# Optimization experiments

Measured on AMD Instinct MI355X. Metric: run time of the kernel, lower is better.

Reference implementation:

```python
import jax, jax.numpy as jnp
import numpy as np

EMBED_DIM = 1024
NUM_HEADS = 16
HEAD_DIM = EMBED_DIM // NUM_HEADS
NUM_GLOBAL = 2
NUM_RANDOM = 3
WINDOW_SIZE = 3
B, S = 2, 2048


def setup_inputs() -> dict:
    key = jax.random.key(0)
    ks = jax.random.split(key, 10)
    scale = 0.02
    inp = {
        "x": jax.random.normal(ks[0], (B, S, EMBED_DIM), dtype=jnp.float32),
        "random_indices": jax.random.randint(ks[1], (S, NUM_RANDOM), 0, S, dtype=jnp.int32),
        "q_w": jax.random.normal(ks[2], (EMBED_DIM, EMBED_DIM), dtype=jnp.float32) * scale,
        "q_b": jnp.zeros((EMBED_DIM,), dtype=jnp.float32),
        "k_w": jax.random.normal(ks[3], (EMBED_DIM, EMBED_DIM), dtype=jnp.float32) * scale,
        "k_b": jnp.zeros((EMBED_DIM,), dtype=jnp.float32),
        "v_w": jax.random.normal(ks[4], (EMBED_DIM, EMBED_DIM), dtype=jnp.float32) * scale,
        "v_b": jnp.zeros((EMBED_DIM,), dtype=jnp.float32),
        "o_w": jax.random.normal(ks[5], (EMBED_DIM, EMBED_DIM), dtype=jnp.float32) * scale,
        "o_b": jnp.zeros((EMBED_DIM,), dtype=jnp.float32),
    }
    return inp


def _build_mask(random_indices, seq_len):
    # [S, S] boolean BigBird mask: global rows/cols + sliding window + random.
    i = jnp.arange(seq_len)[:, None]
    j = jnp.arange(seq_len)[None, :]
    glob = (i < NUM_GLOBAL) | (j < NUM_GLOBAL)
    win = jnp.abs(i - j) <= WINDOW_SIZE
    rand = jnp.zeros((seq_len, seq_len), dtype=bool)
    rows = jnp.repeat(jnp.arange(seq_len), NUM_RANDOM)
    rand = rand.at[rows, random_indices.reshape(-1)].set(True)
    return glob | win | rand


def reference(x, random_indices, q_w, q_b, k_w, k_b, v_w, v_b, o_w, o_b):
    b, s, _ = x.shape
    # torch nn.Linear: y = x @ W.T + b
    q = (x @ q_w.T + q_b).reshape(b, s, NUM_HEADS, HEAD_DIM).transpose(0, 2, 1, 3)
    k = (x @ k_w.T + k_b).reshape(b, s, NUM_HEADS, HEAD_DIM).transpose(0, 2, 1, 3)
    v = (x @ v_w.T + v_b).reshape(b, s, NUM_HEADS, HEAD_DIM).transpose(0, 2, 1, 3)
    scores = jnp.einsum("bhqd,bhkd->bhqk", q, k) / jnp.sqrt(jnp.float32(HEAD_DIM))
    mask = _build_mask(random_indices, s)  # [S, S]
    scores = jnp.where(mask[None, None, :, :], scores, -jnp.inf)
    probs = jax.nn.softmax(scores, axis=-1)
    out = jnp.einsum("bhqk,bhkd->bhqd", probs, v)
    out = out.transpose(0, 2, 1, 3).reshape(b, s, EMBED_DIM)
    return out @ o_w.T + o_b
```

## Files before the change

kernel.cpp:

```cpp
#include <hip/hip_runtime.h>

#define B_  2
#define S_  2048
#define E_  1024
#define H_  16
#define D_  64
#define NGLOB 2
#define NRAND 3
#define WIN 3

typedef __bf16 bf16x8 __attribute__((ext_vector_type(8)));
typedef float  f32x4  __attribute__((ext_vector_type(4)));

__device__ __forceinline__ unsigned short f2bf(float f) {
    unsigned u = __builtin_bit_cast(unsigned, f);
    unsigned r = u + 0x7FFFu + ((u >> 16) & 1u);
    return (unsigned short)(r >> 16);
}
__device__ __forceinline__ float bf2f(unsigned short u) {
    return __builtin_bit_cast(float, (unsigned)u << 16);
}

__device__ __forceinline__ void g2l16(const unsigned short* g, unsigned short* l) {
    __builtin_amdgcn_global_load_lds(
        (const __attribute__((address_space(1))) unsigned*)g,
        (__attribute__((address_space(3))) unsigned*)l, 16, 0, 0);
}

__global__ __launch_bounds__(256)
void convert_all(const float* __restrict__ x,  const float* __restrict__ qw,
                 const float* __restrict__ kw, const float* __restrict__ vw,
                 const float* __restrict__ ow,
                 unsigned short* __restrict__ xb, unsigned short* __restrict__ wqkv,
                 unsigned short* __restrict__ wo) {
    const int XN = (B_ * S_ * E_) / 4;
    const int WN = (E_ * E_) / 4;
    int i = blockIdx.x * blockDim.x + threadIdx.x;
    int r, loc;
    if (i < XN) { r = 0; loc = i; }
    else        { int j = i - XN; r = 1 + (j >> 18); loc = j & (WN - 1); }
    const float* src = r == 0 ? x : r == 1 ? qw : r == 2 ? kw : r == 3 ? vw : ow;
    float4 f = ((const float4*)src)[loc];
    ushort4 u;
    u.x = f2bf(f.x); u.y = f2bf(f.y); u.z = f2bf(f.z); u.w = f2bf(f.w);
    ushort4* dst = r == 0 ? (ushort4*)xb : r == 4 ? (ushort4*)wo
                 : (ushort4*)wqkv + (size_t)(r - 1) * WN;
    dst[loc] = u;
}

__global__ __launch_bounds__(256, 4)
void gemm_qkv(const unsigned short* __restrict__ A,
              const unsigned short* __restrict__ W,
              const float* __restrict__ b0, const float* __restrict__ b1,
              const float* __restrict__ b2,
              unsigned short* __restrict__ Cb, int M, int N, int K) {
    __shared__ unsigned short sA[128 * 64];
    __shared__ unsigned short sB[128 * 64];
    const int t = threadIdx.x;
    const int lane = t & 63;
    const int wave = t >> 6;
    const int wm = wave >> 1, wn = wave & 1;
    const int lq = lane >> 4;
    const int lr = lane & 15;
    const int bm = blockIdx.x * 128;
    const int bn = blockIdx.y * 128;

    f32x4 acc[4][4] = {};

    for (int k0 = 0; k0 < K; k0 += 64) {
        const unsigned short* Abase = A + (size_t)bm * K + k0;
        const unsigned short* Wbase = W + (size_t)bn * K + k0;
        #pragma unroll
        for (int j = 0; j < 4; ++j) {
            int c = j * 256 + t;
            int row = c >> 3, cc = c & 7;
            int gcol = ((cc ^ (row & 7)) << 3);
            int dst = j * 2048 + wave * 512;
            g2l16(Abase + (size_t)row * K + gcol, sA + dst);
            g2l16(Wbase + (size_t)row * K + gcol, sB + dst);
        }
        __syncthreads();

        #pragma unroll
        for (int ks = 0; ks < 2; ++ks) {
            const int sw = (((ks << 2) + lq) ^ (lr & 7)) << 3;
            bf16x8 af[4], bfr[4];
            #pragma unroll
            for (int i = 0; i < 4; ++i)
                af[i] = *(const bf16x8*)&sA[(wm * 64 + i * 16 + lr) * 64 + sw];
            #pragma unroll
            for (int j = 0; j < 4; ++j)
                bfr[j] = *(const bf16x8*)&sB[(wn * 64 + j * 16 + lr) * 64 + sw];
            #pragma unroll
            for (int i = 0; i < 4; ++i)
                #pragma unroll
                for (int j = 0; j < 4; ++j)
                    acc[i][j] = __builtin_amdgcn_mfma_f32_16x16x32_bf16(af[i], bfr[j], acc[i][j], 0, 0, 0);
        }
        __syncthreads();
    }

    #pragma unroll
    for (int i = 0; i < 4; ++i) {
        int row0 = bm + wm * 64 + i * 16 + lq * 4;
        #pragma unroll
        for (int j = 0; j < 4; ++j) {
            int col = bn + wn * 64 + j * 16 + lr;
            const float* bp = col < E_ ? b0 : (col < 2 * E_ ? b1 : b2);
            float bv = bp[col & (E_ - 1)];
            #pragma unroll
            for (int r = 0; r < 4; ++r)
                Cb[(size_t)(row0 + r) * N + col] = f2bf(acc[i][j][r] + bv);
        }
    }
}

__global__ __launch_bounds__(256, 3)
void gemm_o(unsigned short* A,
            const unsigned short* __restrict__ W,
            const float* __restrict__ bias,
            const float* __restrict__ gaccp, const float* __restrict__ gms,
            float* __restrict__ Cf, int M, int N, int K) {
    __shared__ unsigned short sA[128 * 64];
    __shared__ unsigned short sB[128 * 64];
    const int t = threadIdx.x;
    const int lane = t & 63;
    const int wave = t >> 6;
    const int wm = wave >> 1, wn = wave & 1;
    const int lq = lane >> 4;
    const int lr = lane & 15;
    const int bm = blockIdx.x * 128;
    const int bn = blockIdx.y * 128;

    if (blockIdx.x == 0 || blockIdx.x == 16) {
        int b = blockIdx.x >> 4;
        #pragma unroll
        for (int r = 0; r < 8; ++r) {
            int oid = r * 256 + t;
            int i2 = oid >> 10, col = oid & 1023;
            int h = col >> 6, d = col & 63;
            int tup = b * 32 + i2 * 16 + h;
            float Mx = -1e30f;
            #pragma unroll
            for (int c = 0; c < 8; ++c) Mx = fmaxf(Mx, gms[(tup * 8 + c) * 2]);
            float den = 0.f, num = 0.f;
            #pragma unroll
            for (int c = 0; c < 8; ++c) {
                float f = __expf(gms[(tup * 8 + c) * 2] - Mx);
                den += gms[(tup * 8 + c) * 2 + 1] * f;
                num += gaccp[(size_t)(tup * 8 + c) * D_ + d] * f;
            }
            A[(size_t)(b * S_ + i2) * E_ + col] = f2bf(num / den);
        }
        asm volatile("s_waitcnt vmcnt(0)" ::: "memory");
    }
    __syncthreads();

    f32x4 acc[4][4] = {};

    for (int k0 = 0; k0 < K; k0 += 64) {
        const unsigned short* Abase = A + (size_t)bm * K + k0;
        const unsigned short* Wbase = W + (size_t)bn * K + k0;
        #pragma unroll
        for (int j = 0; j < 4; ++j) {
            int c = j * 256 + t;
            int row = c >> 3, cc = c & 7;
            int gcol = ((cc ^ (row & 7)) << 3);
            int dst = j * 2048 + wave * 512;
            g2l16(Abase + (size_t)row * K + gcol, sA + dst);
            g2l16(Wbase + (size_t)row * K + gcol, sB + dst);
        }
        __syncthreads();

        #pragma unroll
        for (int ks = 0; ks < 2; ++ks) {
            const int sw = (((ks << 2) + lq) ^ (lr & 7)) << 3;
            bf16x8 af[4], bfr[4];
            #pragma unroll
            for (int i = 0; i < 4; ++i)
                af[i] = *(const bf16x8*)&sA[(wm * 64 + i * 16 + lr) * 64 + sw];
            #pragma unroll
            for (int j = 0; j < 4; ++j)
                bfr[j] = *(const bf16x8*)&sB[(wn * 64 + j * 16 + lr) * 64 + sw];
            #pragma unroll
            for (int i = 0; i < 4; ++i)
                #pragma unroll
                for (int j = 0; j < 4; ++j)
                    acc[i][j] = __builtin_amdgcn_mfma_f32_16x16x32_bf16(af[i], bfr[j], acc[i][j], 0, 0, 0);
        }
        __syncthreads();
    }

    #pragma unroll
    for (int i = 0; i < 4; ++i) {
        int row0 = bm + wm * 64 + i * 16 + lq * 4;
        #pragma unroll
        for (int j = 0; j < 4; ++j) {
            int col = bn + wn * 64 + j * 16 + lr;
            float bv = bias[col];
            #pragma unroll
            for (int r = 0; r < 4; ++r)
                Cf[(size_t)(row0 + r) * N + col] = acc[i][j][r] + bv;
        }
    }
}

__global__ __launch_bounds__(256)
void attn_fused(const unsigned short* __restrict__ qkv,
                const int* __restrict__ rnd,
                float* __restrict__ gaccp, float* __restrict__ gms,
                unsigned short* __restrict__ attn) {
    const int NB = B_ * (S_ - 2);
    int t = threadIdx.x;

    if (blockIdx.x < 512) {
        int tup = blockIdx.x >> 3, seg = blockIdx.x & 7;
        int b = tup >> 5, i = (tup >> 4) & 1, h = tup & 15;
        int w = t >> 6, l = t & 63;
        __shared__ float redm[4], reds[4];
        __shared__ float ov[4][D_];

        const bf16x8* qp = (const bf16x8*)(qkv + (size_t)(b * S_ + i) * 3072 + h * D_);
        bf16x8 qv = qp[l & 7];
        float qreg[8];
        #pragma unroll
        for (int j = 0; j < 8; ++j) qreg[j] = (float)qv[j];

        const int key0 = seg * 256 + w * 64;
        const int ksb = l >> 3, dg = l & 7;
        float mM = -1e30f, ssum = 0.f;
        float o[8] = {};
        #pragma unroll
        for (int it = 0; it < 8; ++it) {
            int key = key0 + it * 8 + ksb;
            const unsigned short* kr =
                qkv + (size_t)(b * S_ + key) * 3072 + E_ + h * D_ + dg * 8;
            bf16x8 kv = *(const bf16x8*)kr;
            bf16x8 vv = *(const bf16x8*)(kr + E_);
            float s = 0.f;
            #pragma unroll
            for (int j = 0; j < 8; ++j) s += qreg[j] * (float)kv[j];
            s += __shfl_xor(s, 1);
            s += __shfl_xor(s, 2);
            s += __shfl_xor(s, 4);
            s *= 0.125f;
            float m_it = s;
            m_it = fmaxf(m_it, __shfl_xor(m_it, 8));
            m_it = fmaxf(m_it, __shfl_xor(m_it, 16));
            m_it = fmaxf(m_it, __shfl_xor(m_it, 32));
            if (m_it > mM) {
                float r = __expf(mM - m_it);
                ssum *= r;
                #pragma unroll
                for (int e2 = 0; e2 < 8; ++e2) o[e2] *= r;
                mM = m_it;
            }
            float e = __expf(s - mM);
            ssum += e;
            #pragma unroll
            for (int e2 = 0; e2 < 8; ++e2) o[e2] += e * (float)vv[e2];
        }
        #pragma unroll
        for (int mask = 8; mask <= 32; mask <<= 1) {
            ssum += __shfl_xor(ssum, mask);
            #pragma unroll
            for (int e2 = 0; e2 < 8; ++e2) o[e2] += __shfl_xor(o[e2], mask);
        }
        if (l == 0) { redm[w] = mM; reds[w] = ssum; }
        if (ksb == 0)
            #pragma unroll
            for (int e2 = 0; e2 < 8; ++e2) ov[w][dg * 8 + e2] = o[e2];
        __syncthreads();
        if (w == 0) {
            float M = fmaxf(fmaxf(redm[0], redm[1]), fmaxf(redm[2], redm[3]));
            float f0 = __expf(redm[0] - M), f1 = __expf(redm[1] - M);
            float f2 = __expf(redm[2] - M), f3 = __expf(redm[3] - M);
            gaccp[((size_t)tup * 8 + seg) * D_ + l] =
                ov[0][l] * f0 + ov[1][l] * f1 + ov[2][l] * f2 + ov[3][l] * f3;
            if (l == 0) {
                gms[(tup * 8 + seg) * 2]     = M;
                gms[(tup * 8 + seg) * 2 + 1] =
                    reds[0] * f0 + reds[1] * f1 + reds[2] * f2 + reds[3] * f3;
            }
        }
        return;
    }

    int bb = blockIdx.x - 512;
    int bidx = (bb & 7) * 128 + (bb >> 3);
    int w = t >> 6, l = t & 63;
    int row = bidx * 4 + w;
    bool valid = row < NB;
    int b = row / (S_ - 2);
    int i = row % (S_ - 2) + 2;
    if (!valid) { b = 0; i = 2; }

    __shared__ int cols_s[4][12];
    __shared__ int ncol_sh[4];

    const bf16x8* qp = (const bf16x8*)(qkv + (size_t)(b * S_ + i) * 3072);
    bf16x8 q0 = qp[l * 2], q1 = qp[l * 2 + 1];
    float qreg[16];
    #pragma unroll
    for (int j = 0; j < 8; ++j) { qreg[j] = (float)q0[j]; qreg[8 + j] = (float)q1[j]; }

    if (l == 0) {
        int* cols = cols_s[w];
        int n = 0;
        cols[n++] = 0; cols[n++] = 1;
        int lo = i - WIN; if (lo < NGLOB) lo = NGLOB;
        int hi = i + WIN; if (hi > S_ - 1) hi = S_ - 1;
        for (int j = lo; j <= hi; ++j) cols[n++] = j;
        for (int r = 0; r < NRAND; ++r) {
            int c = rnd[i * NRAND + r];
            bool dup = false;
            for (int q = 0; q < n; ++q) dup = dup || (cols[q] == c);
            if (!dup) cols[n++] = c;
        }
        ncol_sh[w] = n;
        for (int q = n; q < 12; ++q) cols[q] = 0;
    }
    __syncthreads();
    const int n = ncol_sh[w];

    float mM = -1e30f, ssum = 0.f;
    float o[16] = {};
    #pragma unroll
    for (int c = 0; c < 12; ++c) {
        const unsigned short* base = qkv + (size_t)(b * S_ + cols_s[w][c]) * 3072 + E_;
        const bf16x8* kp = (const bf16x8*)base;
        bf16x8 k0 = kp[l * 2], k1 = kp[l * 2 + 1];
        const bf16x8* vp = (const bf16x8*)(base + E_);
        bf16x8 v0 = vp[l * 2], v1 = vp[l * 2 + 1];
        float s = 0.f;
        #pragma unroll
        for (int j = 0; j < 8; ++j) s += qreg[j] * (float)k0[j] + qreg[8 + j] * (float)k1[j];
        s += __shfl_xor(s, 1);
        s += __shfl_xor(s, 2);
        s = (c < n) ? s * 0.125f : -1e30f;
        if (s > mM) {
            float r = __expf(mM - s);
            ssum *= r;
            #pragma unroll
            for (int j = 0; j < 16; ++j) o[j] *= r;
            mM = s;
        }
        float e = __expf(s - mM);
        ssum += e;
        #pragma unroll
        for (int j = 0; j < 8; ++j) { o[j] += e * (float)v0[j]; o[8 + j] += e * (float)v1[j]; }
    }
    float inv = 1.f / ssum;
    #pragma unroll
    for (int j = 0; j < 16; ++j) o[j] *= inv;

    if (valid) {
        ushort4 u0, u1, u2, u3;
        u0.x = f2bf(o[0]);  u0.y = f2bf(o[1]);  u0.z = f2bf(o[2]);  u0.w = f2bf(o[3]);
        u1.x = f2bf(o[4]);  u1.y = f2bf(o[5]);  u1.z = f2bf(o[6]);  u1.w = f2bf(o[7]);
        u2.x = f2bf(o[8]);  u2.y = f2bf(o[9]);  u2.z = f2bf(o[10]); u2.w = f2bf(o[11]);
        u3.x = f2bf(o[12]); u3.y = f2bf(o[13]); u3.z = f2bf(o[14]); u3.w = f2bf(o[15]);
        ushort4* op = (ushort4*)(attn + (size_t)(b * S_ + i) * E_ + l * 16);
        op[0] = u0; op[1] = u1; op[2] = u2; op[3] = u3;
    }
}

extern "C" void kernel_launch(void* const* d_in, const int* in_sizes, int n_in,
                              void* d_out, int out_size, void* d_ws, size_t ws_size,
                              hipStream_t stream) {
    const float* x   = (const float*)d_in[0];
    const int*   rnd = (const int*)d_in[1];
    const float* qw  = (const float*)d_in[2];
    const float* qb  = (const float*)d_in[3];
    const float* kw  = (const float*)d_in[4];
    const float* kb  = (const float*)d_in[5];
    const float* vw  = (const float*)d_in[6];
    const float* vb  = (const float*)d_in[7];
    const float* ow  = (const float*)d_in[8];
    const float* ob  = (const float*)d_in[9];
    float* out = (float*)d_out;

    char* ws = (char*)d_ws;
    unsigned short* xb    = (unsigned short*)(ws);
    unsigned short* wqkv  = (unsigned short*)(ws + 8388608);
    unsigned short* wo    = (unsigned short*)(ws + 14680064);
    unsigned short* qkv   = (unsigned short*)(ws + 16777216);
    unsigned short* attn  = (unsigned short*)(ws + 41943040);
    float*          gaccp = (float*)(ws);
    float*          gms   = (float*)(ws + 131072);

    const int M = B_ * S_;

    {
        int total4 = (M * E_ + 4 * E_ * E_) / 4;
        convert_all<<<total4 / 256, 256, 0, stream>>>(x, qw, kw, vw, ow, xb, wqkv, wo);
    }

    {
        dim3 grid(M / 128, 3 * E_ / 128);
        gemm_qkv<<<grid, 256, 0, stream>>>(xb, wqkv, qb, kb, vb, qkv, M, 3 * E_, E_);
    }

    attn_fused<<<512 + 1024, 256, 0, stream>>>(qkv, rnd, gaccp, gms, attn);

    {
        dim3 grid(M / 128, E_ / 128);
        gemm_o<<<grid, 256, 0, stream>>>(attn, wo, ob, gaccp, gms, out, M, E_, E_);
    }
}
```

Before: 160.1 us.

## Split attention key loops across two wavefronts per row with LDS merge

Doubles the attention block to 512 threads. Global-query blocks now have each wave cover 32 keys instead of 64, and the results of 8 waves are merged. Sparse rows are now handled by two waves, each processing half of the 12 candidate columns, with the partial softmax states combined through shared memory. This shortens each wave's serial latency-bound loop and exposes more memory parallelism, at the cost of an extra LDS round trip, a barrier, and more threads per block.

```diff
diff --git a/kernel.cpp b/kernel.cpp
--- a/kernel.cpp
+++ b/kernel.cpp
@@ -205,20 +205,20 @@
     }
 }
 
-__global__ __launch_bounds__(256)
+__global__ __launch_bounds__(512)
 void attn_fused(const unsigned short* __restrict__ qkv,
                 const int* __restrict__ rnd,
                 float* __restrict__ gaccp, float* __restrict__ gms,
                 unsigned short* __restrict__ attn) {
     const int NB = B_ * (S_ - 2);
     int t = threadIdx.x;
+    int w = t >> 6, l = t & 63;
 
     if (blockIdx.x < 512) {
         int tup = blockIdx.x >> 3, seg = blockIdx.x & 7;
         int b = tup >> 5, i = (tup >> 4) & 1, h = tup & 15;
-        int w = t >> 6, l = t & 63;
-        __shared__ float redm[4], reds[4];
-        __shared__ float ov[4][D_];
+        __shared__ float redm[8], reds[8];
+        __shared__ float ov[8][D_];
 
         const bf16x8* qp = (const bf16x8*)(qkv + (size_t)(b * S_ + i) * 3072 + h * D_);
         bf16x8 qv = qp[l & 7];
@@ -226,12 +226,12 @@
         #pragma unroll
         for (int j = 0; j < 8; ++j) qreg[j] = (float)qv[j];
 
-        const int key0 = seg * 256 + w * 64;
+        const int key0 = seg * 256 + w * 32;
         const int ksb = l >> 3, dg = l & 7;
         float mM = -1e30f, ssum = 0.f;
         float o[8] = {};
         #pragma unroll
-        for (int it = 0; it < 8; ++it) {
+        for (int it = 0; it < 4; ++it) {
             int key = key0 + it * 8 + ksb;
             const unsigned short* kr =
                 qkv + (size_t)(b * S_ + key) * 3072 + E_ + h * D_ + dg * 8;
@@ -272,15 +272,20 @@
             for (int e2 = 0; e2 < 8; ++e2) ov[w][dg * 8 + e2] = o[e2];
         __syncthreads();
         if (w == 0) {
-            float M = fmaxf(fmaxf(redm[0], redm[1]), fmaxf(redm[2], redm[3]));
-            float f0 = __expf(redm[0] - M), f1 = __expf(redm[1] - M);
-            float f2 = __expf(redm[2] - M), f3 = __expf(redm[3] - M);
-            gaccp[((size_t)tup * 8 + seg) * D_ + l] =
-                ov[0][l] * f0 + ov[1][l] * f1 + ov[2][l] * f2 + ov[3][l] * f3;
+            float M = -1e30f;
+            #pragma unroll
+            for (int ww = 0; ww < 8; ++ww) M = fmaxf(M, redm[ww]);
+            float num = 0.f, den = 0.f;
+            #pragma unroll
+            for (int ww = 0; ww < 8; ++ww) {
+                float f = __expf(redm[ww] - M);
+                num += ov[ww][l] * f;
+                den += reds[ww] * f;
+            }
+            gaccp[((size_t)tup * 8 + seg) * D_ + l] = num;
             if (l == 0) {
                 gms[(tup * 8 + seg) * 2]     = M;
-                gms[(tup * 8 + seg) * 2 + 1] =
-                    reds[0] * f0 + reds[1] * f1 + reds[2] * f2 + reds[3] * f3;
+                gms[(tup * 8 + seg) * 2 + 1] = den;
             }
         }
         return;
@@ -288,15 +293,17 @@
 
     int bb = blockIdx.x - 512;
     int bidx = (bb & 7) * 128 + (bb >> 3);
-    int w = t >> 6, l = t & 63;
-    int row = bidx * 4 + w;
+    int r = w >> 1, half = w & 1;
+    int row = bidx * 4 + r;
     bool valid = row < NB;
     int b = row / (S_ - 2);
     int i = row % (S_ - 2) + 2;
     if (!valid) { b = 0; i = 2; }
 
-    __shared__ int cols_s[4][12];
-    __shared__ int ncol_sh[4];
+    __shared__ int   cols_s[4][12];
+    __shared__ int   ncol_sh[4];
+    __shared__ float mh[4][2][16], sh[4][2][16];
+    __shared__ float oh[4][2][64][17];
 
     const bf16x8* qp = (const bf16x8*)(qkv + (size_t)(b * S_ + i) * 3072);
     bf16x8 q0 = qp[l * 2], q1 = qp[l * 2 + 1];
@@ -304,30 +311,31 @@
     #pragma unroll
     for (int j = 0; j < 8; ++j) { qreg[j] = (float)q0[j]; qreg[8 + j] = (float)q1[j]; }
 
-    if (l == 0) {
-        int* cols = cols_s[w];
+    if (half == 0 && l == 0) {
+        int* cols = cols_s[r];
         int n = 0;
         cols[n++] = 0; cols[n++] = 1;
         int lo = i - WIN; if (lo < NGLOB) lo = NGLOB;
         int hi = i + WIN; if (hi > S_ - 1) hi = S_ - 1;
         for (int j = lo; j <= hi; ++j) cols[n++] = j;
-        for (int r = 0; r < NRAND; ++r) {
-            int c = rnd[i * NRAND + r];
+        for (int q = 0; q < NRAND; ++q) {
+            int c = rnd[i * NRAND + q];
             bool dup = false;
-            for (int q = 0; q < n; ++q) dup = dup || (cols[q] == c);
+            for (int p = 0; p < n; ++p) dup = dup || (cols[p] == c);
             if (!dup) cols[n++] = c;
         }
-        ncol_sh[w] = n;
+        ncol_sh[r] = n;
         for (int q = n; q < 12; ++q) cols[q] = 0;
     }
     __syncthreads();
-    const int n = ncol_sh[w];
+    const int n = ncol_sh[r];
 
     float mM = -1e30f, ssum = 0.f;
     float o[16] = {};
     #pragma unroll
-    for (int c = 0; c < 12; ++c) {
-        const unsigned short* base = qkv + (size_t)(b * S_ + cols_s[w][c]) * 3072 + E_;
+    for (int j6 = 0; j6 < 6; ++j6) {
+        int c = half * 6 + j6;
+        const unsigned short* base = qkv + (size_t)(b * S_ + cols_s[r][c]) * 3072 + E_;
         const bf16x8* kp = (const bf16x8*)base;
         bf16x8 k0 = kp[l * 2], k1 = kp[l * 2 + 1];
         const bf16x8* vp = (const bf16x8*)(base + E_);
@@ -337,29 +345,43 @@
         for (int j = 0; j < 8; ++j) s += qreg[j] * (float)k0[j] + qreg[8 + j] * (float)k1[j];
         s += __shfl_xor(s, 1);
         s += __shfl_xor(s, 2);
-        s = (c < n) ? s * 0.125f : -1e30f;
+        bool ok = (c < n);
+        s = ok ? s * 0.125f : -1e30f;
         if (s > mM) {
-            float r = __expf(mM - s);
-            ssum *= r;
-            #pragma unroll
-            for (int j = 0; j < 16; ++j) o[j] *= r;
+            float rr = __expf(mM - s);
+            ssum *= rr;
+            #pragma unroll
+            for (int j = 0; j < 16; ++j) o[j] *= rr;
             mM = s;
         }
-        float e = __expf(s - mM);
+        float e = ok ? __expf(s - mM) : 0.f;
         ssum += e;
         #pragma unroll
         for (int j = 0; j < 8; ++j) { o[j] += e * (float)v0[j]; o[8 + j] += e * (float)v1[j]; }
     }
-    float inv = 1.f / ssum;
+
+    if ((l & 3) == 0) { mh[r][half][l >> 2] = mM; sh[r][half][l >> 2] = ssum; }
     #pragma unroll
-    for (int j = 0; j < 16; ++j) o[j] *= inv;
-
-    if (valid) {
+    for (int j = 0; j < 16; ++j) oh[r][half][l][j] = o[j];
+    __syncthreads();
+
+    if (half == 0 && valid) {
+        int h4 = l >> 2;
+        float m0 = mh[r][0][h4], m1 = mh[r][1][h4];
+        float M = fmaxf(m0, m1);
+        float f0 = __expf(m0 - M), f1 = __expf(m1 - M);
+        float den = sh[r][0][h4] * f0 + sh[r][1][h4] * f1;
+        float inv = 1.f / den;
+        float oc[16];
+        #pragma unroll
+        for (int j = 0; j < 16; ++j)
+            oc[j] = (o[j] * f0 + oh[r][1][l][j] * f1) * inv;
+
         ushort4 u0, u1, u2, u3;
-        u0.x = f2bf(o[0]);  u0.y = f2bf(o[1]);  u0.z = f2bf(o[2]);  u0.w = f2bf(o[3]);
-        u1.x = f2bf(o[4]);  u1.y = f2bf(o[5]);  u1.z = f2bf(o[6]);  u1.w = f2bf(o[7]);
-        u2.x = f2bf(o[8]);  u2.y = f2bf(o[9]);  u2.z = f2bf(o[10]); u2.w = f2bf(o[11]);
-        u3.x = f2bf(o[12]); u3.y = f2bf(o[13]); u3.z = f2bf(o[14]); u3.w = f2bf(o[15]);
+        u0.x = f2bf(oc[0]);  u0.y = f2bf(oc[1]);  u0.z = f2bf(oc[2]);  u0.w = f2bf(oc[3]);
+        u1.x = f2bf(oc[4]);  u1.y = f2bf(oc[5]);  u1.z = f2bf(oc[6]);  u1.w = f2bf(oc[7]);
+        u2.x = f2bf(oc[8]);  u2.y = f2bf(oc[9]);  u2.z = f2bf(oc[10]); u2.w = f2bf(oc[11]);
+        u3.x = f2bf(oc[12]); u3.y = f2bf(oc[13]); u3.z = f2bf(oc[14]); u3.w = f2bf(oc[15]);
         ushort4* op = (ushort4*)(attn + (size_t)(b * S_ + i) * E_ + l * 16);
         op[0] = u0; op[1] = u1; op[2] = u2; op[3] = u3;
     }
@@ -401,7 +423,7 @@
         gemm_qkv<<<grid, 256, 0, stream>>>(xb, wqkv, qb, kb, vb, qkv, M, 3 * E_, E_);
     }
 
-    attn_fused<<<512 + 1024, 256, 0, stream>>>(qkv, rnd, gaccp, gms, attn);
+    attn_fused<<<512 + 1024, 512, 0, stream>>>(qkv, rnd, gaccp, gms, attn);
 
     {
         dim3 grid(M / 128, E_ / 128);
```

Measured after the change: 163.4 us. 1.02x slower.
